# Performance work log

Measured on AMD Instinct MI355X. Metric: run time of the kernel, lower is better.

Reference implementation:

```python
import jax, jax.numpy as jnp
import numpy as np

C = 1024
H = C // 64          # 16 heads
CH = 64              # head dim
NUM_BUCKETS = 32
MAX_DISTANCE = 64
REL_SCALE = float(np.sqrt(CH))  # (channels//num_heads)**0.5 = 8
EPS = 1e-5


def group_norm(x, gamma, beta, groups):
    # x: [B, C, T]
    B, Cc, T = x.shape
    xg = x.reshape(B, groups, -1)
    m = xg.mean(-1, keepdims=True)
    v = xg.var(-1, keepdims=True)
    xn = ((xg - m) * jax.lax.rsqrt(v + EPS)).reshape(B, Cc, T)
    return xn * gamma[None, :, None] + beta[None, :, None]


def conv1d(x, w, b, pad):
    # x: [B, Cin, T], w: [Cout, Cin, K]
    y = jax.lax.conv_general_dilated(x, w, (1,), [(pad, pad)],
                                     dimension_numbers=('NCH', 'OIH', 'NCH'))
    return y + b[None, :, None]


def rel_pos_bias(T, emb):
    # lucidrains RelativePositionBias, non-causal; emb: [num_buckets, H]
    pos = jnp.arange(T)
    n = pos[:, None] - pos[None, :]          # n = -(k - q) = q - k
    half = NUM_BUCKETS // 2                  # 16
    ret = (n < 0).astype(jnp.int32) * half
    n = jnp.abs(n)
    max_exact = half // 2                    # 8
    is_small = n < max_exact
    nf = jnp.maximum(n, 1).astype(jnp.float32)
    val_large = max_exact + (jnp.log(nf / max_exact)
                             / np.log(MAX_DISTANCE / max_exact)
                             * (half - max_exact)).astype(jnp.int32)
    val_large = jnp.minimum(val_large, half - 1)
    bucket = ret + jnp.where(is_small, n, val_large)  # [T, T]
    return emb[bucket].transpose(2, 0, 1)             # [H, T, T]


def setup_inputs() -> dict:
    key = jax.random.key(0)
    ks = jax.random.split(key, 20)
    B, T = 8, 1024
    s = 0.02
    return {
        'x': jax.random.normal(ks[0], (B, C, T), jnp.float32),
        # ResBlock in_layers
        'rb_gn1_g': jnp.ones((C,), jnp.float32),
        'rb_gn1_b': jnp.zeros((C,), jnp.float32),
        'rb_conv1_w': jax.random.normal(ks[1], (C, C, 3), jnp.float32) * s,
        'rb_conv1_b': jnp.zeros((C,), jnp.float32),
        # ResBlock out_layers (zero-init in original; randomized for testing)
        'rb_gn2_g': jnp.ones((C,), jnp.float32),
        'rb_gn2_b': jnp.zeros((C,), jnp.float32),
        'rb_conv2_w': jax.random.normal(ks[2], (C, C, 3), jnp.float32) * s,
        'rb_conv2_b': jnp.zeros((C,), jnp.float32),
        # outer GroupNorm(8, C)
        'norm_g': jnp.ones((C,), jnp.float32),
        'norm_b': jnp.zeros((C,), jnp.float32),
        # AttentionBlock
        'attn_gn_g': jnp.ones((C,), jnp.float32),
        'attn_gn_b': jnp.zeros((C,), jnp.float32),
        'qkv_w': jax.random.normal(ks[3], (3 * C, C, 1), jnp.float32) * s,
        'qkv_b': jnp.zeros((3 * C,), jnp.float32),
        'proj_w': jax.random.normal(ks[4], (C, C, 1), jnp.float32) * s,
        'proj_b': jnp.zeros((C,), jnp.float32),
        'rel_emb': jax.random.normal(ks[5], (NUM_BUCKETS, H), jnp.float32) * s,
    }


def reference(x, rb_gn1_g, rb_gn1_b, rb_conv1_w, rb_conv1_b,
              rb_gn2_g, rb_gn2_b, rb_conv2_w, rb_conv2_b,
              norm_g, norm_b, attn_gn_g, attn_gn_b,
              qkv_w, qkv_b, proj_w, proj_b, rel_emb):
    B, Cc, T = x.shape
    # ResBlock: GN32 -> SiLU -> conv3 -> GN32 -> SiLU -> (dropout=0) -> conv3, + skip
    h = jax.nn.silu(group_norm(x, rb_gn1_g, rb_gn1_b, 32))
    h = conv1d(h, rb_conv1_w, rb_conv1_b, 1)
    h = jax.nn.silu(group_norm(h, rb_gn2_g, rb_gn2_b, 32))
    h = conv1d(h, rb_conv2_w, rb_conv2_b, 1)
    h = x + h
    # outer GroupNorm(8)
    h = group_norm(h, norm_g, norm_b, 8)
    # AttentionBlock with relative position bias
    xin = h
    qkv = conv1d(group_norm(h, attn_gn_g, attn_gn_b, 32), qkv_w, qkv_b, 0)
    # channel layout after reshape(bs*H, 3*ch, T): [H, 3, ch]
    qkv = qkv.reshape(B, H, 3, CH, T)
    q, k, v = qkv[:, :, 0], qkv[:, :, 1], qkv[:, :, 2]
    scale = CH ** -0.25
    w = jnp.einsum('bhct,bhcs->bhts', q * scale, k * scale)
    bias = rel_pos_bias(T, rel_emb) * REL_SCALE       # [H, T, T]
    w = jax.nn.softmax((w + bias[None]).astype(jnp.float32), axis=-1).astype(w.dtype)
    a = jnp.einsum('bhts,bhcs->bhct', w, v).reshape(B, Cc, T)
    return xin + conv1d(a, proj_w, proj_b, 0)
```

## Files before the change

kernel.cpp:

```cpp
#include <hip/hip_runtime.h>

typedef __attribute__((ext_vector_type(4))) float f32x4;
typedef __attribute__((ext_vector_type(8))) __bf16 bf16x8;
typedef __attribute__((ext_vector_type(4))) unsigned short us4;
typedef __attribute__((ext_vector_type(8))) unsigned short us8;

#define DEVI static __device__ __forceinline__

DEVI unsigned short f2bf(float f){
  union { float f; unsigned u; } x; x.f = f;
  unsigned r = x.u + 0x7fffu + ((x.u >> 16) & 1u);
  return (unsigned short)(r >> 16);
}
DEVI float bf2f(unsigned short h){
  union { unsigned u; float f; } x; x.u = ((unsigned)h) << 16;
  return x.f;
}

typedef __attribute__((address_space(1))) unsigned int gu32;
typedef __attribute__((address_space(3))) unsigned int lu32;
DEVI void gll16(const void* g, void* l){
  __builtin_amdgcn_global_load_lds((gu32*)g, (lu32*)l, 16, 0, 0);
}

DEVI f32x4 mfma16(bf16x8 a, bf16x8 b, f32x4 c){
  return __builtin_amdgcn_mfma_f32_16x16x32_bf16(a, b, c, 0, 0, 0);
}

DEVI float wredsum(float v){
  #pragma unroll
  for (int m = 1; m < 64; m <<= 1) v += __shfl_xor(v, m);
  return v;
}

__global__ __launch_bounds__(256) void conv_w_prep(const float* __restrict__ w,
                                                   unsigned short* __restrict__ wp){
  int idx = blockIdx.x * 256 + threadIdx.x;
  const float* p = w + (size_t)idx * 3;
  wp[idx]           = f2bf(p[0]);
  wp[1048576 + idx] = f2bf(p[1]);
  wp[2097152 + idx] = f2bf(p[2]);
}

__global__ __launch_bounds__(256) void cast_f2b(const float* __restrict__ in,
                                                unsigned short* __restrict__ out, int n4){
  int idx = blockIdx.x * 256 + threadIdx.x;
  if (idx < n4){
    f32x4 v = *(const f32x4*)&in[(size_t)idx * 4];
    us4 o;
    #pragma unroll
    for (int j = 0; j < 4; j++) o[j] = f2bf(v[j]);
    *(us4*)&out[(size_t)idx * 4] = o;
  }
}

__global__ __launch_bounds__(256) void btab_k(const float* __restrict__ emb,
                                              float* __restrict__ btab){
  int idx = blockIdx.x * 256 + threadIdx.x;
  if (idx >= 2047 * 16) return;
  int d = idx >> 4, h = idx & 15;
  int n0 = d - 1023;
  int ret = (n0 < 0) ? 16 : 0;
  int n = (n0 < 0) ? -n0 : n0;
  int bucket;
  if (n < 8) bucket = ret + n;
  else {
    float ratio = logf((float)n * 0.125f) / 2.0794415416798357f;
    int vl = 8 + (int)(ratio * 8.0f);
    bucket = ret + (vl < 15 ? vl : 15);
  }
  btab[h * 2048 + d] = emb[bucket * 16 + h] * 11.541560327111707f;
}

__global__ __launch_bounds__(256) void zero_pads(unsigned short* __restrict__ h1p,
                                                 unsigned short* __restrict__ g2p){
  int idx = blockIdx.x * 256 + threadIdx.x;
  int b = idx >> 11, rr = (idx >> 10) & 1, c = idx & 1023;
  size_t off = ((size_t)b * 1026 + (rr ? 1025 : 0)) * 1024 + c;
  h1p[off] = 0; g2p[off] = 0;
}

__global__ __launch_bounds__(256) void gn_stats_f32(const float* __restrict__ in,
                                                    float2* __restrict__ st){
  const int g = blockIdx.x; const int tid = threadIdx.x;
  const float* p = in + (size_t)g * 32768;
  float s = 0.f, s2 = 0.f;
  for (int i = tid * 4; i < 32768; i += 1024){
    f32x4 v = *(const f32x4*)&p[i];
    #pragma unroll
    for (int j = 0; j < 4; j++){ s += v[j]; s2 += v[j] * v[j]; }
  }
  s = wredsum(s); s2 = wredsum(s2);
  __shared__ float rs[4], rs2[4];
  if ((tid & 63) == 0){ rs[tid >> 6] = s; rs2[tid >> 6] = s2; }
  __syncthreads();
  if (tid == 0){
    float S = rs[0] + rs[1] + rs[2] + rs[3];
    float S2 = rs2[0] + rs2[1] + rs2[2] + rs2[3];
    float m = S * (1.f / 32768.f);
    float var = S2 * (1.f / 32768.f) - m * m;
    st[g] = make_float2(m, rsqrtf(var + 1e-5f));
  }
}

__global__ __launch_bounds__(256) void gn_stats_bf16(const unsigned short* __restrict__ in,
                                                     float2* __restrict__ st){
  const int g = blockIdx.x; const int tid = threadIdx.x;
  const unsigned short* p = in + (size_t)g * 32768;
  float s = 0.f, s2 = 0.f;
  for (int i = tid * 8; i < 32768; i += 2048){
    us8 v = *(const us8*)&p[i];
    #pragma unroll
    for (int j = 0; j < 8; j++){ float f = bf2f(v[j]); s += f; s2 += f * f; }
  }
  s = wredsum(s); s2 = wredsum(s2);
  __shared__ float rs[4], rs2[4];
  if ((tid & 63) == 0){ rs[tid >> 6] = s; rs2[tid >> 6] = s2; }
  __syncthreads();
  if (tid == 0){
    float S = rs[0] + rs[1] + rs[2] + rs[3];
    float S2 = rs2[0] + rs2[1] + rs2[2] + rs2[3];
    float m = S * (1.f / 32768.f);
    float var = S2 * (1.f / 32768.f) - m * m;
    st[g] = make_float2(m, rsqrtf(var + 1e-5f));
  }
}

template<int SILU, int INBF16, int OUTPAD>
__global__ __launch_bounds__(256) void gn_apply_tr(
    const void* __restrict__ inp, const float2* __restrict__ st,
    const float* __restrict__ gma, const float* __restrict__ bta,
    unsigned short* __restrict__ out)
{
  const int gid = blockIdx.x;
  const int tc = gid & 15, g = (gid >> 4) & 31, b = gid >> 9;
  const int tid = threadIdx.x;
  const int t0 = tc * 64;
  __shared__ __align__(16) unsigned short tr[64 * 40];
  float2 s = st[b * 32 + g];
  int c = tid >> 3, t8 = (tid & 7) * 8;
  int ch = g * 32 + c;
  float sc = gma[ch] * s.y;
  float sh = bta[ch] - s.x * sc;
  float vv[8];
  if (INBF16){
    const unsigned short* p = (const unsigned short*)inp + ((size_t)b * 1024 + ch) * 1024 + t0 + t8;
    us8 v = *(const us8*)p;
    #pragma unroll
    for (int j = 0; j < 8; j++) vv[j] = bf2f(v[j]);
  } else {
    const float* p = (const float*)inp + ((size_t)b * 1024 + ch) * 1024 + t0 + t8;
    f32x4 v0 = *(const f32x4*)p; f32x4 v1 = *(const f32x4*)(p + 4);
    #pragma unroll
    for (int j = 0; j < 4; j++){ vv[j] = v0[j]; vv[4 + j] = v1[j]; }
  }
  #pragma unroll
  for (int j = 0; j < 8; j++){
    float v = vv[j] * sc + sh;
    if (SILU) v = v / (1.f + __expf(-v));
    tr[(t8 + j) * 40 + c] = f2bf(v);
  }
  __syncthreads();
  int t = tid >> 2, c8 = (tid & 3) * 8;
  us8 d = *(const us8*)&tr[t * 40 + c8];
  size_t row = OUTPAD ? ((size_t)b * 1026 + 1 + t0 + t) : ((size_t)b * 1024 + t0 + t);
  *(us8*)&out[row * 1024 + g * 32 + c8] = d;
}

__global__ __launch_bounds__(256) void gn2_partial(const unsigned short* __restrict__ c1,
                                                   float2* __restrict__ part){
  const int tid = threadIdx.x;
  const int ck = blockIdx.x & 31, b = blockIdx.x >> 5;
  const unsigned short* p = c1 + ((size_t)b * 1024 + ck * 32) * 1024 + tid * 4;
  float s = 0.f, s2 = 0.f;
  for (int r = 0; r < 32; r++){
    us4 v = *(const us4*)&p[(size_t)r * 1024];
    #pragma unroll
    for (int j = 0; j < 4; j++){ float f = bf2f(v[j]); s += f; s2 += f * f; }
  }
  __shared__ float ls[256], ls2[256];
  ls[tid] = s; ls2[tid] = s2;
  __syncthreads();
  if (tid < 32){
    float S = 0.f, S2 = 0.f;
    #pragma unroll
    for (int k = 0; k < 8; k++){ S += ls[tid * 8 + k]; S2 += ls2[tid * 8 + k]; }
    part[((size_t)b * 32 + ck) * 32 + tid] = make_float2(S, S2);
  }
}

template<int SILU>
__global__ __launch_bounds__(256) void gn2_apply(const unsigned short* __restrict__ c1,
    const float2* __restrict__ part, const float* __restrict__ gma, const float* __restrict__ bta,
    unsigned short* __restrict__ outp)
{
  const int tid = threadIdx.x;
  const int ck = blockIdx.x & 31, b = blockIdx.x >> 5;
  __shared__ float2 st[32];
  if (tid < 32){
    float S = 0.f, S2 = 0.f;
    for (int k = 0; k < 32; k++){ float2 pp = part[((size_t)b * 32 + k) * 32 + tid]; S += pp.x; S2 += pp.y; }
    float m = S * (1.f / 32768.f);
    float var = S2 * (1.f / 32768.f) - m * m;
    st[tid] = make_float2(m, rsqrtf(var + 1e-5f));
  }
  __syncthreads();
  float2 s = st[tid >> 3];
  float sc[4], sh[4];
  #pragma unroll
  for (int j = 0; j < 4; j++){ int ch = tid * 4 + j; sc[j] = gma[ch] * s.y; sh[j] = bta[ch] - s.x * sc[j]; }
  const unsigned short* p = c1 + ((size_t)b * 1024 + ck * 32) * 1024 + tid * 4;
  unsigned short* q = outp + ((size_t)b * 1026 + 1 + ck * 32) * 1024 + tid * 4;
  for (int r = 0; r < 32; r++){
    us4 v = *(const us4*)&p[(size_t)r * 1024];
    us4 o;
    #pragma unroll
    for (int j = 0; j < 4; j++){
      float f = bf2f(v[j]) * sc[j] + sh[j];
      if (SILU) f = f / (1.f + __expf(-f));
      o[j] = f2bf(f);
    }
    *(us4*)&q[(size_t)r * 1024] = o;
  }
}

__global__ __launch_bounds__(256) void gn8_partial(const float* __restrict__ r,
                                                   float2* __restrict__ part){
  const int gid = blockIdx.x; const int tid = threadIdx.x;
  const int sub = gid & 15, g = (gid >> 4) & 7, b = gid >> 7;
  const float* p = r + ((size_t)(b * 8 + g)) * 131072 + sub * 8192;
  float s = 0.f, s2 = 0.f;
  for (int i = tid * 8; i < 8192; i += 2048){
    f32x4 v0 = *(const f32x4*)&p[i], v1 = *(const f32x4*)&p[i + 4];
    #pragma unroll
    for (int j = 0; j < 4; j++){ s += v0[j] + v1[j]; s2 += v0[j] * v0[j] + v1[j] * v1[j]; }
  }
  s = wredsum(s); s2 = wredsum(s2);
  __shared__ float rs[4], rs2[4];
  if ((tid & 63) == 0){ rs[tid >> 6] = s; rs2[tid >> 6] = s2; }
  __syncthreads();
  if (tid == 0) part[gid] = make_float2(rs[0] + rs[1] + rs[2] + rs[3],
                                        rs2[0] + rs2[1] + rs2[2] + rs2[3]);
}

__global__ __launch_bounds__(256) void gn8_apply(const float* __restrict__ r,
    const float2* __restrict__ part, const float* __restrict__ gma, const float* __restrict__ bta,
    unsigned short* __restrict__ xin){
  const int gid = blockIdx.x; const int tid = threadIdx.x;
  const int sub = gid & 15, g = (gid >> 4) & 7, b = gid >> 7;
  __shared__ float2 stt;
  if (tid == 0){
    float S = 0.f, S2 = 0.f;
    #pragma unroll
    for (int k = 0; k < 16; k++){ float2 pp = part[(gid & ~15) + k]; S += pp.x; S2 += pp.y; }
    float m = S * (1.f / 131072.f);
    float var = S2 * (1.f / 131072.f) - m * m;
    stt = make_float2(m, rsqrtf(var + 1e-5f));
  }
  __syncthreads();
  float2 s = stt;
  const float* pr = r + ((size_t)(b * 8 + g)) * 131072 + sub * 8192;
  unsigned short* px = xin + ((size_t)(b * 8 + g)) * 131072 + sub * 8192;
  for (int i = tid * 8; i < 8192; i += 2048){
    int c = g * 128 + sub * 8 + (i >> 10);
    float sc = gma[c] * s.y, sh = bta[c] - s.x * sc;
    f32x4 v0 = *(const f32x4*)&pr[i], v1 = *(const f32x4*)&pr[i + 4];
    us8 o;
    #pragma unroll
    for (int j = 0; j < 4; j++){ o[j] = f2bf(v0[j] * sc + sh); o[4 + j] = f2bf(v1[j] * sc + sh); }
    *(us8*)&px[i] = o;
  }
}

template<int KK, int EPI>
__global__ __launch_bounds__(256, 2) void gemm_k(
    const unsigned short* __restrict__ inT,
    const unsigned short* __restrict__ W,
    const float* __restrict__ bias,
    void* __restrict__ outp,
    void* __restrict__ resp,
    int OC, int NT)
{
  __shared__ __align__(16) unsigned short Alds[128 * 64];
  __shared__ __align__(16) unsigned short Blds[128 * 64];
  const int tid = threadIdx.x;
  const int lane = tid & 63;
  const int w = tid >> 6;
  const int wn = w >> 1, wo = w & 1;
  const int nt = blockIdx.x % NT;
  const int ot = blockIdx.x / NT;
  const int b = nt >> 3;
  const int t0 = (nt & 7) * 128;
  const int ob = ot * 128;
  const int rowbase = (KK == 3) ? (b * 1026 + t0) : (b * 1024 + t0);

  f32x4 acc[4][4];
  #pragma unroll
  for (int m = 0; m < 4; m++)
    #pragma unroll
    for (int n = 0; n < 4; n++) acc[m][n] = 0.f;

  const int lrow = lane >> 3;
  const int lblk = lane & 7;

  for (int kk = 0; kk < KK; ++kk){
    const unsigned short* Ab = inT + (size_t)(rowbase + kk) * 1024;
    const unsigned short* Bb = W + ((size_t)kk * OC + ob) * 1024;
    for (int i0 = 0; i0 < 1024; i0 += 64){
      #pragma unroll
      for (int j = 0; j < 4; ++j){
        int chunk = w * 4 + j;
        int row = chunk * 8 + lrow;
        int gcol = (lblk ^ (row & 7)) * 8;
        gll16(Ab + (size_t)row * 1024 + i0 + gcol, &Alds[chunk * 512]);
        gll16(Bb + (size_t)row * 1024 + i0 + gcol, &Blds[chunk * 512]);
      }
      __syncthreads();
      bf16x8 af[2][4], bfv[2][4];
      #pragma unroll
      for (int m = 0; m < 4; m++){
        int row = wn * 64 + m * 16 + (lane & 15);
        #pragma unroll
        for (int k2 = 0; k2 < 2; k2++){
          int blk = ((lane >> 4) + k2 * 4) ^ (row & 7);
          af[k2][m] = *(const bf16x8*)&Alds[row * 64 + blk * 8];
        }
      }
      #pragma unroll
      for (int n = 0; n < 4; n++){
        int row = wo * 64 + n * 16 + (lane & 15);
        #pragma unroll
        for (int k2 = 0; k2 < 2; k2++){
          int blk = ((lane >> 4) + k2 * 4) ^ (row & 7);
          bfv[k2][n] = *(const bf16x8*)&Blds[row * 64 + blk * 8];
        }
      }
      #pragma unroll
      for (int k2 = 0; k2 < 2; k2++)
        #pragma unroll
        for (int m = 0; m < 4; m++)
          #pragma unroll
          for (int n = 0; n < 4; n++)
            acc[m][n] = mfma16(af[k2][m], bfv[k2][n], acc[m][n]);
      __syncthreads();
    }
  }

  if (EPI == 0){
    unsigned short* out = (unsigned short*)outp;
    #pragma unroll
    for (int m = 0; m < 4; m++){
      int tl = t0 + wn * 64 + m * 16 + ((lane >> 4) * 4);
      #pragma unroll
      for (int n = 0; n < 4; n++){
        int o = ob + wo * 64 + n * 16 + (lane & 15);
        float bz = bias[o];
        size_t base = ((size_t)b * 1024 + tl) * OC + o;
        #pragma unroll
        for (int r = 0; r < 4; r++)
          out[base + (size_t)r * OC] = f2bf(acc[m][n][r] + bz);
      }
    }
  } else if (EPI == 3){
    unsigned short* qkT = (unsigned short*)outp;
    unsigned short* vT  = (unsigned short*)resp;
    #pragma unroll
    for (int m = 0; m < 4; m++){
      int tl = t0 + wn * 64 + m * 16 + ((lane >> 4) * 4);
      #pragma unroll
      for (int n = 0; n < 4; n++){
        int o0 = ob + wo * 64 + n * 16;
        int h = o0 / 192;
        int rem0 = o0 - h * 192;
        int o = o0 + (lane & 15);
        float bz = bias[o];
        if (rem0 < 128){
          size_t base = ((size_t)b * 1024 + tl) * 2048 + h * 128 + rem0 + (lane & 15);
          #pragma unroll
          for (int r = 0; r < 4; r++)
            qkT[base + (size_t)r * 2048] = f2bf(acc[m][n][r] + bz);
        } else {
          int c = rem0 - 128 + (lane & 15);
          size_t base = (((size_t)(b * 16 + h)) * 64 + c) * 1024 + tl;
          us4 o4;
          #pragma unroll
          for (int r = 0; r < 4; r++) o4[r] = f2bf(acc[m][n][r] + bz);
          *(us4*)&vT[base] = o4;
        }
      }
    }
  } else {
    float* out = (float*)outp;
    #pragma unroll
    for (int m = 0; m < 4; m++){
      int tl = t0 + wn * 64 + m * 16 + ((lane >> 4) * 4);
      #pragma unroll
      for (int n = 0; n < 4; n++){
        int o = ob + wo * 64 + n * 16 + (lane & 15);
        float bz = bias[o];
        size_t base = ((size_t)b * 1024 + o) * 1024 + tl;
        f32x4 v;
        if (EPI == 1){
          const float* xr = (const float*)resp;
          v = *(const f32x4*)&xr[base];
        } else {
          const unsigned short* xr = (const unsigned short*)resp;
          us4 xv = *(const us4*)&xr[base];
          v[0] = bf2f(xv[0]); v[1] = bf2f(xv[1]); v[2] = bf2f(xv[2]); v[3] = bf2f(xv[3]);
        }
        #pragma unroll
        for (int r = 0; r < 4; r++) v[r] += acc[m][n][r] + bz;
        *(f32x4*)&out[base] = v;
      }
    }
  }
}

__global__ __launch_bounds__(256, 2) void attn_k4(
    const unsigned short* __restrict__ qkT,
    const unsigned short* __restrict__ vT,
    const float* __restrict__ btab,
    unsigned short* __restrict__ aT)
{
  __shared__ __align__(16) unsigned short Kb[2][64 * 64];
  __shared__ __align__(16) unsigned short Vb[2][64 * 64];
  __shared__ __align__(16) unsigned short Pb[4][32 * 64];
  __shared__ __align__(16) float blds[1152];
  const int tid = threadIdx.x, lane = tid & 63, w = tid >> 6;
  const int d0 = blockIdx.x;
  const int xcd = d0 & 7, slot = d0 >> 3;
  const int bh = xcd * 16 + (slot >> 3);
  const int qt = slot & 7;
  const int h = bh & 15, b = bh >> 4;
  const int q0b = qt * 128;
  const int q0 = q0b + w * 32;
  const unsigned short* qk = qkT + (size_t)b * 1024 * 2048 + h * 128;
  const unsigned short* vh = vT + ((size_t)(b * 16 + h)) * 64 * 1024;
  const int lc = lane & 15, lg = lane >> 4;

  for (int i = tid; i < 1151; i += 256)
    blds[i] = btab[h * 2048 + q0b + i];

  bf16x8 qf[2][2];
  #pragma unroll
  for (int m = 0; m < 2; m++){
    const unsigned short* qrow = qk + (size_t)(q0 + m * 16 + lc) * 2048;
    #pragma unroll
    for (int k2 = 0; k2 < 2; k2++)
      qf[m][k2] = *(const bf16x8*)&qrow[k2 * 32 + lg * 8];
  }
  float m_run[2], l_run[2];
  f32x4 oacc[2][4];
  m_run[0] = m_run[1] = -1e30f; l_run[0] = l_run[1] = 0.f;
  #pragma unroll
  for (int m = 0; m < 2; m++)
    #pragma unroll
    for (int cb = 0; cb < 4; cb++) oacc[m][cb] = 0.f;

  const int lr = lane >> 3, lb = lane & 7;
  const float qs = 0.18033688011112042f;

  #pragma unroll
  for (int j = 0; j < 2; j++){
    int chunk = w * 2 + j;
    int row = chunk * 8 + lr;
    int gcol = (lb ^ (row & 7)) * 8;
    gll16(qk + 64 + (size_t)row * 2048 + gcol, &Kb[0][chunk * 512]);
    gll16(vh + (size_t)row * 1024 + gcol, &Vb[0][chunk * 512]);
  }
  __syncthreads();

  for (int t = 0; t < 16; ++t){
    const int cur = t & 1;
    const int st0 = t * 64;
    if (t < 15){
      int nst = st0 + 64;
      #pragma unroll
      for (int j = 0; j < 2; j++){
        int chunk = w * 2 + j;
        int row = chunk * 8 + lr;
        int gcol = (lb ^ (row & 7)) * 8;
        gll16(qk + 64 + (size_t)(nst + row) * 2048 + gcol, &Kb[cur ^ 1][chunk * 512]);
        gll16(vh + (size_t)row * 1024 + nst + gcol, &Vb[cur ^ 1][chunk * 512]);
      }
    }
    f32x4 sfr[2][4];
    #pragma unroll
    for (int m = 0; m < 2; m++)
      #pragma unroll
      for (int sub = 0; sub < 4; sub++) sfr[m][sub] = 0.f;
    __builtin_amdgcn_s_setprio(1);
    #pragma unroll
    for (int sub = 0; sub < 4; sub++){
      int row = sub * 16 + lc;
      #pragma unroll
      for (int k2 = 0; k2 < 2; k2++){
        int blk = (lg + k2 * 4) ^ (row & 7);
        bf16x8 bk = *(const bf16x8*)&Kb[cur][row * 64 + blk * 8];
        sfr[0][sub] = mfma16(bk, qf[0][k2], sfr[0][sub]);
        sfr[1][sub] = mfma16(bk, qf[1][k2], sfr[1][sub]);
      }
    }
    __builtin_amdgcn_s_setprio(0);
    float pm2[2];
    #pragma unroll
    for (int m = 0; m < 2; m++){
      const float* bp = &blds[(w * 32 + m * 16 + lc) + 960 - st0];
      #pragma unroll
      for (int sub = 0; sub < 4; sub++){
        int off = 63 - sub * 16 - lg * 4;
        #pragma unroll
        for (int r = 0; r < 4; r++)
          sfr[m][sub][r] = sfr[m][sub][r] * qs + bp[off - r];
      }
      float x0 = fmaxf(fmaxf(sfr[m][0][0], sfr[m][0][1]), fmaxf(sfr[m][0][2], sfr[m][0][3]));
      float x1 = fmaxf(fmaxf(sfr[m][1][0], sfr[m][1][1]), fmaxf(sfr[m][1][2], sfr[m][1][3]));
      float x2 = fmaxf(fmaxf(sfr[m][2][0], sfr[m][2][1]), fmaxf(sfr[m][2][2], sfr[m][2][3]));
      float x3 = fmaxf(fmaxf(sfr[m][3][0], sfr[m][3][1]), fmaxf(sfr[m][3][2], sfr[m][3][3]));
      float pm = fmaxf(fmaxf(x0, x1), fmaxf(x2, x3));
      pm = fmaxf(pm, __shfl_xor(pm, 16));
      pm = fmaxf(pm, __shfl_xor(pm, 32));
      pm2[m] = pm;
    }
    bool stable = (pm2[0] <= m_run[0] + 8.f) && (pm2[1] <= m_run[1] + 8.f);
    if (__all(stable)){
      #pragma unroll
      for (int m = 0; m < 2; m++){
        float ssum = 0.f;
        #pragma unroll
        for (int sub = 0; sub < 4; sub++)
          #pragma unroll
          for (int r = 0; r < 4; r++){
            float e = exp2f(sfr[m][sub][r] - m_run[m]);
            sfr[m][sub][r] = e;
            ssum += e;
          }
        ssum += __shfl_xor(ssum, 16);
        ssum += __shfl_xor(ssum, 32);
        l_run[m] += ssum;
      }
    } else {
      float corr[2];
      #pragma unroll
      for (int m = 0; m < 2; m++){
        float mn = fmaxf(m_run[m], pm2[m]);
        corr[m] = exp2f(m_run[m] - mn);
        m_run[m] = mn;
        float ssum = 0.f;
        #pragma unroll
        for (int sub = 0; sub < 4; sub++)
          #pragma unroll
          for (int r = 0; r < 4; r++){
            float e = exp2f(sfr[m][sub][r] - mn);
            sfr[m][sub][r] = e;
            ssum += e;
          }
        ssum += __shfl_xor(ssum, 16);
        ssum += __shfl_xor(ssum, 32);
        l_run[m] = l_run[m] * corr[m] + ssum;
      }
      #pragma unroll
      for (int m = 0; m < 2; m++)
        #pragma unroll
        for (int r = 0; r < 4; r++){
          float co = __shfl(corr[m], lg * 4 + r);
          #pragma unroll
          for (int cb = 0; cb < 4; cb++) oacc[m][cb][r] *= co;
        }
    }
    unsigned short* P = &Pb[w][0];
    #pragma unroll
    for (int m = 0; m < 2; m++){
      int qrow = m * 16 + lc;
      int rsw = (qrow & 7) << 3;
      #pragma unroll
      for (int sub = 0; sub < 4; sub++){
        int col = sub * 16 + lg * 4;
        unsigned w0, w1;
        asm("v_cvt_pk_bf16_f32 %0, %1, %2" : "=v"(w0) : "v"(sfr[m][sub][0]), "v"(sfr[m][sub][1]));
        asm("v_cvt_pk_bf16_f32 %0, %1, %2" : "=v"(w1) : "v"(sfr[m][sub][2]), "v"(sfr[m][sub][3]));
        uint2 pk; pk.x = w0; pk.y = w1;
        *(uint2*)&P[qrow * 64 + (col ^ rsw)] = pk;
      }
    }
    __builtin_amdgcn_s_setprio(1);
    #pragma unroll
    for (int k2 = 0; k2 < 2; k2++){
      bf16x8 pa[2];
      #pragma unroll
      for (int m = 0; m < 2; m++){
        int rowp = m * 16 + lc;
        int blkp = (lg + k2 * 4) ^ (rowp & 7);
        pa[m] = *(const bf16x8*)&P[rowp * 64 + blkp * 8];
      }
      #pragma unroll
      for (int cb = 0; cb < 4; cb++){
        int ch = cb * 16 + lc;
        int blkv = (lg + k2 * 4) ^ (ch & 7);
        bf16x8 bv = *(const bf16x8*)&Vb[cur][ch * 64 + blkv * 8];
        oacc[0][cb] = mfma16(pa[0], bv, oacc[0][cb]);
        oacc[1][cb] = mfma16(pa[1], bv, oacc[1][cb]);
      }
    }
    __builtin_amdgcn_s_setprio(0);
    __syncthreads();
  }
  #pragma unroll
  for (int m = 0; m < 2; m++)
    #pragma unroll
    for (int r = 0; r < 4; r++){
      float li = 1.0f / __shfl(l_run[m], lg * 4 + r);
      int tq = q0 + m * 16 + lg * 4 + r;
      #pragma unroll
      for (int cb = 0; cb < 4; cb++){
        int ch = h * 64 + cb * 16 + lc;
        aT[((size_t)b * 1024 + tq) * 1024 + ch] = f2bf(oacc[m][cb][r] * li);
      }
    }
}

extern "C" void kernel_launch(void* const* d_in, const int* in_sizes, int n_in,
                              void* d_out, int out_size, void* d_ws, size_t ws_size,
                              hipStream_t stream)
{
  const float* x       = (const float*)d_in[0];
  const float* gn1_g   = (const float*)d_in[1];
  const float* gn1_b   = (const float*)d_in[2];
  const float* conv1_w = (const float*)d_in[3];
  const float* conv1_b = (const float*)d_in[4];
  const float* gn2_g   = (const float*)d_in[5];
  const float* gn2_b   = (const float*)d_in[6];
  const float* conv2_w = (const float*)d_in[7];
  const float* conv2_b = (const float*)d_in[8];
  const float* norm_g  = (const float*)d_in[9];
  const float* norm_b  = (const float*)d_in[10];
  const float* agn_g   = (const float*)d_in[11];
  const float* agn_b   = (const float*)d_in[12];
  const float* qkv_w   = (const float*)d_in[13];
  const float* qkv_b   = (const float*)d_in[14];
  const float* proj_w  = (const float*)d_in[15];
  const float* proj_b  = (const float*)d_in[16];
  const float* rel_emb = (const float*)d_in[17];

  if (ws_size < 139526144u) return;

  char* ws = (char*)d_ws;
  unsigned short* w1p   = (unsigned short*)(ws + 0);
  unsigned short* w2p   = (unsigned short*)(ws + 6291456);
  unsigned short* wqkv  = (unsigned short*)(ws + 12582912);
  unsigned short* wproj = (unsigned short*)(ws + 18874368);
  float* btab           = (float*)(ws + 20971520);
  float2* stats1        = (float2*)(ws + 21102592);
  float2* part2         = (float2*)(ws + 21104640);
  float2* stats32       = (float2*)(ws + 21170176);
  float2* part8         = (float2*)(ws + 21172224);
  unsigned short* h1p   = (unsigned short*)(ws + 22020096);
  unsigned short* c1    = (unsigned short*)(ws + 38830080);
  unsigned short* g2p   = (unsigned short*)(ws + 55607296);
  unsigned short* qkT   = h1p;
  unsigned short* vT    = (unsigned short*)(ws + 55574528);
  float* rbuf           = (float*)(ws + 72417280);
  unsigned short* attn_in = (unsigned short*)(ws + 72417280);
  unsigned short* xin   = (unsigned short*)(ws + 105971712);
  unsigned short* aT    = (unsigned short*)(ws + 122748928);

  conv_w_prep<<<4096, 256, 0, stream>>>(conv1_w, w1p);
  conv_w_prep<<<4096, 256, 0, stream>>>(conv2_w, w2p);
  cast_f2b<<<3072, 256, 0, stream>>>(qkv_w, wqkv, 3072 * 1024 / 4);
  cast_f2b<<<1024, 256, 0, stream>>>(proj_w, wproj, 1024 * 1024 / 4);
  btab_k<<<128, 256, 0, stream>>>(rel_emb, btab);
  zero_pads<<<64, 256, 0, stream>>>(h1p, g2p);

  gn_stats_f32<<<256, 256, 0, stream>>>(x, stats1);
  gn_apply_tr<1, 0, 1><<<4096, 256, 0, stream>>>(x, stats1, gn1_g, gn1_b, h1p);

  gemm_k<3, 0><<<512, 256, 0, stream>>>(h1p, w1p, conv1_b, c1, nullptr, 1024, 64);

  gn2_partial<<<256, 256, 0, stream>>>(c1, part2);
  gn2_apply<1><<<256, 256, 0, stream>>>(c1, part2, gn2_g, gn2_b, g2p);

  gemm_k<3, 1><<<512, 256, 0, stream>>>(g2p, w2p, conv2_b, rbuf, (void*)x, 1024, 64);

  gn8_partial<<<1024, 256, 0, stream>>>(rbuf, part8);
  gn8_apply<<<1024, 256, 0, stream>>>(rbuf, part8, norm_g, norm_b, xin);

  gn_stats_bf16<<<256, 256, 0, stream>>>(xin, stats32);
  gn_apply_tr<0, 1, 0><<<4096, 256, 0, stream>>>(xin, stats32, agn_g, agn_b, attn_in);

  gemm_k<1, 3><<<1536, 256, 0, stream>>>(attn_in, wqkv, qkv_b, qkT, vT, 3072, 64);

  attn_k4<<<1024, 256, 0, stream>>>(qkT, vT, btab, aT);

  gemm_k<1, 2><<<512, 256, 0, stream>>>(aT, wproj, proj_b, d_out, xin, 1024, 64);
}
```

Before: 390.4 us.

## Keep residual stream in bf16 and skip bias gather on uniform-bucket attention tiles

The GN1 stats kernel now also writes a bf16 copy of x. The conv2 GEMM reads that copy as the residual and writes its sum back in bf16 instead of fp32, and the GN8 kernels read bf16, which roughly halves traffic for that intermediate. In the attention kernel, key tiles whose relative distances all land in the saturated bucket use a single constant bias folded into the exp2 argument, avoiding the per-element LDS bias adds. The cost is extra bf16 rounding of the residual path before GroupNorm8.

```diff
diff --git a/kernel.cpp b/kernel.cpp
--- a/kernel.cpp
+++ b/kernel.cpp
@@ -80,15 +80,19 @@
   h1p[off] = 0; g2p[off] = 0;
 }
 
-__global__ __launch_bounds__(256) void gn_stats_f32(const float* __restrict__ in,
-                                                    float2* __restrict__ st){
+__global__ __launch_bounds__(256) void gn_stats_cast(const float* __restrict__ in,
+                                                     float2* __restrict__ st,
+                                                     unsigned short* __restrict__ xb){
   const int g = blockIdx.x; const int tid = threadIdx.x;
   const float* p = in + (size_t)g * 32768;
+  unsigned short* q = xb + (size_t)g * 32768;
   float s = 0.f, s2 = 0.f;
   for (int i = tid * 4; i < 32768; i += 1024){
     f32x4 v = *(const f32x4*)&p[i];
-    #pragma unroll
-    for (int j = 0; j < 4; j++){ s += v[j]; s2 += v[j] * v[j]; }
+    us4 o;
+    #pragma unroll
+    for (int j = 0; j < 4; j++){ s += v[j]; s2 += v[j] * v[j]; o[j] = f2bf(v[j]); }
+    *(us4*)&q[i] = o;
   }
   s = wredsum(s); s2 = wredsum(s2);
   __shared__ float rs[4], rs2[4];
@@ -224,16 +228,16 @@
   }
 }
 
-__global__ __launch_bounds__(256) void gn8_partial(const float* __restrict__ r,
+__global__ __launch_bounds__(256) void gn8_partial(const unsigned short* __restrict__ r,
                                                    float2* __restrict__ part){
   const int gid = blockIdx.x; const int tid = threadIdx.x;
   const int sub = gid & 15, g = (gid >> 4) & 7, b = gid >> 7;
-  const float* p = r + ((size_t)(b * 8 + g)) * 131072 + sub * 8192;
+  const unsigned short* p = r + ((size_t)(b * 8 + g)) * 131072 + sub * 8192;
   float s = 0.f, s2 = 0.f;
   for (int i = tid * 8; i < 8192; i += 2048){
-    f32x4 v0 = *(const f32x4*)&p[i], v1 = *(const f32x4*)&p[i + 4];
-    #pragma unroll
-    for (int j = 0; j < 4; j++){ s += v0[j] + v1[j]; s2 += v0[j] * v0[j] + v1[j] * v1[j]; }
+    us8 v = *(const us8*)&p[i];
+    #pragma unroll
+    for (int j = 0; j < 8; j++){ float f = bf2f(v[j]); s += f; s2 += f * f; }
   }
   s = wredsum(s); s2 = wredsum(s2);
   __shared__ float rs[4], rs2[4];
@@ -243,7 +247,7 @@
                                         rs2[0] + rs2[1] + rs2[2] + rs2[3]);
 }
 
-__global__ __launch_bounds__(256) void gn8_apply(const float* __restrict__ r,
+__global__ __launch_bounds__(256) void gn8_apply(const unsigned short* __restrict__ r,
     const float2* __restrict__ part, const float* __restrict__ gma, const float* __restrict__ bta,
     unsigned short* __restrict__ xin){
   const int gid = blockIdx.x; const int tid = threadIdx.x;
@@ -259,15 +263,15 @@
   }
   __syncthreads();
   float2 s = stt;
-  const float* pr = r + ((size_t)(b * 8 + g)) * 131072 + sub * 8192;
+  const unsigned short* pr = r + ((size_t)(b * 8 + g)) * 131072 + sub * 8192;
   unsigned short* px = xin + ((size_t)(b * 8 + g)) * 131072 + sub * 8192;
   for (int i = tid * 8; i < 8192; i += 2048){
     int c = g * 128 + sub * 8 + (i >> 10);
     float sc = gma[c] * s.y, sh = bta[c] - s.x * sc;
-    f32x4 v0 = *(const f32x4*)&pr[i], v1 = *(const f32x4*)&pr[i + 4];
+    us8 v = *(const us8*)&pr[i];
     us8 o;
     #pragma unroll
-    for (int j = 0; j < 4; j++){ o[j] = f2bf(v0[j] * sc + sh); o[4 + j] = f2bf(v1[j] * sc + sh); }
+    for (int j = 0; j < 8; j++) o[j] = f2bf(bf2f(v[j]) * sc + sh);
     *(us8*)&px[i] = o;
   }
 }
@@ -389,8 +393,9 @@
         }
       }
     }
-  } else {
-    float* out = (float*)outp;
+  } else if (EPI == 4){
+    unsigned short* out = (unsigned short*)outp;
+    const unsigned short* xr = (const unsigned short*)resp;
     #pragma unroll
     for (int m = 0; m < 4; m++){
       int tl = t0 + wn * 64 + m * 16 + ((lane >> 4) * 4);
@@ -399,15 +404,27 @@
         int o = ob + wo * 64 + n * 16 + (lane & 15);
         float bz = bias[o];
         size_t base = ((size_t)b * 1024 + o) * 1024 + tl;
+        us4 xv = *(const us4*)&xr[base];
+        us4 ov;
+        #pragma unroll
+        for (int r = 0; r < 4; r++) ov[r] = f2bf(bf2f(xv[r]) + acc[m][n][r] + bz);
+        *(us4*)&out[base] = ov;
+      }
+    }
+  } else {
+    float* out = (float*)outp;
+    #pragma unroll
+    for (int m = 0; m < 4; m++){
+      int tl = t0 + wn * 64 + m * 16 + ((lane >> 4) * 4);
+      #pragma unroll
+      for (int n = 0; n < 4; n++){
+        int o = ob + wo * 64 + n * 16 + (lane & 15);
+        float bz = bias[o];
+        size_t base = ((size_t)b * 1024 + o) * 1024 + tl;
+        const unsigned short* xr = (const unsigned short*)resp;
+        us4 xv = *(const us4*)&xr[base];
         f32x4 v;
-        if (EPI == 1){
-          const float* xr = (const float*)resp;
-          v = *(const f32x4*)&xr[base];
-        } else {
-          const unsigned short* xr = (const unsigned short*)resp;
-          us4 xv = *(const us4*)&xr[base];
-          v[0] = bf2f(xv[0]); v[1] = bf2f(xv[1]); v[2] = bf2f(xv[2]); v[3] = bf2f(xv[3]);
-        }
+        v[0] = bf2f(xv[0]); v[1] = bf2f(xv[1]); v[2] = bf2f(xv[2]); v[3] = bf2f(xv[3]);
         #pragma unroll
         for (int r = 0; r < 4; r++) v[r] += acc[m][n][r] + bz;
         *(f32x4*)&out[base] = v;
@@ -416,7 +433,7 @@
   }
 }
 
-__global__ __launch_bounds__(256, 2) void attn_k4(
+__global__ __launch_bounds__(256, 2) void attn_k5(
     const unsigned short* __restrict__ qkT,
     const unsigned short* __restrict__ vT,
     const float* __restrict__ btab,
@@ -438,6 +455,9 @@
   const unsigned short* vh = vT + ((size_t)(b * 16 + h)) * 64 * 1024;
   const int lc = lane & 15, lg = lane >> 4;
 
+  const float bneg = btab[h * 2048 + 0];
+  const float bpos = btab[h * 2048 + 2046];
+
   for (int i = tid; i < 1151; i += 256)
     blds[i] = btab[h * 2048 + q0b + i];
 
@@ -502,63 +522,73 @@
       }
     }
     __builtin_amdgcn_s_setprio(0);
+    const bool unineg = (st0 >= q0 + 81);
+    const bool unipos = (st0 + 113 <= q0);
+    const bool uni = unineg || unipos;
+    const float bc = unineg ? bneg : bpos;
     float pm2[2];
-    #pragma unroll
-    for (int m = 0; m < 2; m++){
-      const float* bp = &blds[(w * 32 + m * 16 + lc) + 960 - st0];
-      #pragma unroll
-      for (int sub = 0; sub < 4; sub++){
-        int off = 63 - sub * 16 - lg * 4;
-        #pragma unroll
-        for (int r = 0; r < 4; r++)
-          sfr[m][sub][r] = sfr[m][sub][r] * qs + bp[off - r];
-      }
-      float x0 = fmaxf(fmaxf(sfr[m][0][0], sfr[m][0][1]), fmaxf(sfr[m][0][2], sfr[m][0][3]));
-      float x1 = fmaxf(fmaxf(sfr[m][1][0], sfr[m][1][1]), fmaxf(sfr[m][1][2], sfr[m][1][3]));
-      float x2 = fmaxf(fmaxf(sfr[m][2][0], sfr[m][2][1]), fmaxf(sfr[m][2][2], sfr[m][2][3]));
-      float x3 = fmaxf(fmaxf(sfr[m][3][0], sfr[m][3][1]), fmaxf(sfr[m][3][2], sfr[m][3][3]));
-      float pm = fmaxf(fmaxf(x0, x1), fmaxf(x2, x3));
-      pm = fmaxf(pm, __shfl_xor(pm, 16));
-      pm = fmaxf(pm, __shfl_xor(pm, 32));
-      pm2[m] = pm;
-    }
-    bool stable = (pm2[0] <= m_run[0] + 8.f) && (pm2[1] <= m_run[1] + 8.f);
-    if (__all(stable)){
+    if (uni){
       #pragma unroll
       for (int m = 0; m < 2; m++){
-        float ssum = 0.f;
-        #pragma unroll
-        for (int sub = 0; sub < 4; sub++)
+        float x0 = fmaxf(fmaxf(sfr[m][0][0], sfr[m][0][1]), fmaxf(sfr[m][0][2], sfr[m][0][3]));
+        float x1 = fmaxf(fmaxf(sfr[m][1][0], sfr[m][1][1]), fmaxf(sfr[m][1][2], sfr[m][1][3]));
+        float x2 = fmaxf(fmaxf(sfr[m][2][0], sfr[m][2][1]), fmaxf(sfr[m][2][2], sfr[m][2][3]));
+        float x3 = fmaxf(fmaxf(sfr[m][3][0], sfr[m][3][1]), fmaxf(sfr[m][3][2], sfr[m][3][3]));
+        float pm = fmaxf(fmaxf(x0, x1), fmaxf(x2, x3)) * qs + bc;
+        pm = fmaxf(pm, __shfl_xor(pm, 16));
+        pm = fmaxf(pm, __shfl_xor(pm, 32));
+        pm2[m] = pm;
+      }
+    } else {
+      #pragma unroll
+      for (int m = 0; m < 2; m++){
+        const float* bp = &blds[(w * 32 + m * 16 + lc) + 960 - st0];
+        #pragma unroll
+        for (int sub = 0; sub < 4; sub++){
+          int off = 63 - sub * 16 - lg * 4;
           #pragma unroll
-          for (int r = 0; r < 4; r++){
-            float e = exp2f(sfr[m][sub][r] - m_run[m]);
-            sfr[m][sub][r] = e;
-            ssum += e;
-          }
-        ssum += __shfl_xor(ssum, 16);
-        ssum += __shfl_xor(ssum, 32);
-        l_run[m] += ssum;
-      }
-    } else {
-      float corr[2];
+          for (int r = 0; r < 4; r++)
+            sfr[m][sub][r] = sfr[m][sub][r] * qs + bp[off - r];
+        }
+        float x0 = fmaxf(fmaxf(sfr[m][0][0], sfr[m][0][1]), fmaxf(sfr[m][0][2], sfr[m][0][3]));
+        float x1 = fmaxf(fmaxf(sfr[m][1][0], sfr[m][1][1]), fmaxf(sfr[m][1][2], sfr[m][1][3]));
+        float x2 = fmaxf(fmaxf(sfr[m][2][0], sfr[m][2][1]), fmaxf(sfr[m][2][2], sfr[m][2][3]));
+        float x3 = fmaxf(fmaxf(sfr[m][3][0], sfr[m][3][1]), fmaxf(sfr[m][3][2], sfr[m][3][3]));
+        float pm = fmaxf(fmaxf(x0, x1), fmaxf(x2, x3));
+        pm = fmaxf(pm, __shfl_xor(pm, 16));
+        pm = fmaxf(pm, __shfl_xor(pm, 32));
+        pm2[m] = pm;
+      }
+    }
+    const bool stable = (pm2[0] <= m_run[0] + 8.f) && (pm2[1] <= m_run[1] + 8.f);
+    const bool resc = !__all(stable);
+    float corr[2], mref[2];
+    if (resc){
       #pragma unroll
       for (int m = 0; m < 2; m++){
         float mn = fmaxf(m_run[m], pm2[m]);
         corr[m] = exp2f(m_run[m] - mn);
-        m_run[m] = mn;
-        float ssum = 0.f;
-        #pragma unroll
-        for (int sub = 0; sub < 4; sub++)
-          #pragma unroll
-          for (int r = 0; r < 4; r++){
-            float e = exp2f(sfr[m][sub][r] - mn);
-            sfr[m][sub][r] = e;
-            ssum += e;
-          }
-        ssum += __shfl_xor(ssum, 16);
-        ssum += __shfl_xor(ssum, 32);
-        l_run[m] = l_run[m] * corr[m] + ssum;
-      }
+        m_run[m] = mn; mref[m] = mn;
+      }
+    } else { mref[0] = m_run[0]; mref[1] = m_run[1]; }
+    const float scl = uni ? qs : 1.f;
+    #pragma unroll
+    for (int m = 0; m < 2; m++){
+      const float ad = (uni ? bc : 0.f) - mref[m];
+      float ssum = 0.f;
+      #pragma unroll
+      for (int sub = 0; sub < 4; sub++)
+        #pragma unroll
+        for (int r = 0; r < 4; r++){
+          float e = exp2f(fmaf(sfr[m][sub][r], scl, ad));
+          sfr[m][sub][r] = e;
+          ssum += e;
+        }
+      ssum += __shfl_xor(ssum, 16);
+      ssum += __shfl_xor(ssum, 32);
+      l_run[m] = resc ? (l_run[m] * corr[m] + ssum) : (l_run[m] + ssum);
+    }
+    if (resc){
       #pragma unroll
       for (int m = 0; m < 2; m++)
         #pragma unroll
@@ -659,7 +689,7 @@
   unsigned short* g2p   = (unsigned short*)(ws + 55607296);
   unsigned short* qkT   = h1p;
   unsigned short* vT    = (unsigned short*)(ws + 55574528);
-  float* rbuf           = (float*)(ws + 72417280);
+  unsigned short* xb    = (unsigned short*)(ws + 72417280);
   unsigned short* attn_in = (unsigned short*)(ws + 72417280);
   unsigned short* xin   = (unsigned short*)(ws + 105971712);
   unsigned short* aT    = (unsigned short*)(ws + 122748928);
@@ -671,7 +701,7 @@
   btab_k<<<128, 256, 0, stream>>>(rel_emb, btab);
   zero_pads<<<64, 256, 0, stream>>>(h1p, g2p);
 
-  gn_stats_f32<<<256, 256, 0, stream>>>(x, stats1);
+  gn_stats_cast<<<256, 256, 0, stream>>>(x, stats1, xb);
   gn_apply_tr<1, 0, 1><<<4096, 256, 0, stream>>>(x, stats1, gn1_g, gn1_b, h1p);
 
   gemm_k<3, 0><<<512, 256, 0, stream>>>(h1p, w1p, conv1_b, c1, nullptr, 1024, 64);
@@ -679,17 +709,17 @@
   gn2_partial<<<256, 256, 0, stream>>>(c1, part2);
   gn2_apply<1><<<256, 256, 0, stream>>>(c1, part2, gn2_g, gn2_b, g2p);
 
-  gemm_k<3, 1><<<512, 256, 0, stream>>>(g2p, w2p, conv2_b, rbuf, (void*)x, 1024, 64);
-
-  gn8_partial<<<1024, 256, 0, stream>>>(rbuf, part8);
-  gn8_apply<<<1024, 256, 0, stream>>>(rbuf, part8, norm_g, norm_b, xin);
+  gemm_k<3, 4><<<512, 256, 0, stream>>>(g2p, w2p, conv2_b, xb, xb, 1024, 64);
+
+  gn8_partial<<<1024, 256, 0, stream>>>(xb, part8);
+  gn8_apply<<<1024, 256, 0, stream>>>(xb, part8, norm_g, norm_b, xin);
 
   gn_stats_bf16<<<256, 256, 0, stream>>>(xin, stats32);
   gn_apply_tr<0, 1, 0><<<4096, 256, 0, stream>>>(xin, stats32, agn_g, agn_b, attn_in);
 
   gemm_k<1, 3><<<1536, 256, 0, stream>>>(attn_in, wqkv, qkv_b, qkT, vT, 3072, 64);
 
-  attn_k4<<<1024, 256, 0, stream>>>(qkT, vT, btab, aT);
+  attn_k5<<<1024, 256, 0, stream>>>(qkT, vT, btab, aT);
 
   gemm_k<1, 2><<<512, 256, 0, stream>>>(aT, wproj, proj_b, d_out, xin, 1024, 64);
 }
```

Measured after the change: 381.0 us. 2.4% less time.
